# Optimization experiments

Hardware: AMD Instinct MI355X
Metric: run time of the kernel (lower is better)

## Reference

```python
import jax, jax.numpy as jnp
import numpy as np

N_NODES = 100000
N_EDGES = 1600000
N_GRAPHS = 512
NEG_SLOPE = 0.2  # PyG GATConv default


def setup_inputs() -> dict:
    key = jax.random.key(0)
    ks = jax.random.split(key, 12)
    x = jax.random.normal(ks[0], (N_NODES, 75), dtype=jnp.float32)
    edge_index = jax.random.randint(ks[1], (2, N_EDGES), 0, N_NODES, dtype=jnp.int64 if jax.config.jax_enable_x64 else jnp.int32)
    batch = jnp.sort(jax.random.randint(ks[2], (N_NODES,), 0, N_GRAPHS, dtype=jnp.int32))
    s = lambda k, shp, fan: jax.random.normal(k, shp, dtype=jnp.float32) * (1.0 / np.sqrt(fan))
    return {
        "x": x, "edge_index": edge_index, "batch": batch,
        "W1": s(ks[3], (75, 64), 75),           # conv1: heads=8, out=8
        "att_src1": s(ks[4], (8, 8), 8),
        "att_dst1": s(ks[5], (8, 8), 8),
        "bias1": jnp.zeros((64,), jnp.float32),
        "W2": s(ks[6], (64, 128), 64),          # conv2: heads=1, out=128
        "att_src2": s(ks[7], (1, 128), 128),
        "att_dst2": s(ks[8], (1, 128), 128),
        "bias2": jnp.zeros((128,), jnp.float32),
        "Wg": s(ks[9], (128, 1), 128),
        "bg": jnp.zeros((1,), jnp.float32),
    }


def _gat_conv(x, src, dst, W, att_src, att_dst, bias, heads, out_ch):
    # x: [N, F_in]; edges src->dst (self-loops already included)
    n = x.shape[0]
    h = (x @ W).reshape(n, heads, out_ch)            # [N, H, C]
    a_src = (h * att_src).sum(-1)                    # [N, H]
    a_dst = (h * att_dst).sum(-1)                    # [N, H]
    e = a_src[src] + a_dst[dst]                      # [E, H]
    e = jax.nn.leaky_relu(e, NEG_SLOPE)
    # segment softmax over incoming edges of each dst node
    emax = jax.ops.segment_max(e, dst, num_segments=n)      # [N, H]
    ee = jnp.exp(e - emax[dst])
    denom = jax.ops.segment_sum(ee, dst, num_segments=n)    # [N, H]
    alpha = ee / denom[dst]                                  # [E, H]
    msg = h[src] * alpha[:, :, None]                          # [E, H, C]
    out = jax.ops.segment_sum(msg, dst, num_segments=n)      # [N, H, C]
    return out.reshape(n, heads * out_ch) + bias


def reference(x, edge_index, batch, W1, att_src1, att_dst1, bias1,
              W2, att_src2, att_dst2, bias2, Wg, bg):
    n = x.shape[0]
    # PyG GATConv adds self-loops by default
    loops = jnp.arange(n, dtype=edge_index.dtype)
    src = jnp.concatenate([edge_index[0], loops])
    dst = jnp.concatenate([edge_index[1], loops])
    # eval mode: dropout is identity
    x2 = jax.nn.elu(_gat_conv(x, src, dst, W1, att_src1, att_dst1, bias1, heads=8, out_ch=8))
    x4 = _gat_conv(x2, src, dst, W2, att_src2, att_dst2, bias2, heads=1, out_ch=128)
    y = jax.ops.segment_sum(x4, batch, num_segments=N_GRAPHS)  # global_add_pool
    return y @ Wg + bg  # [N_GRAPHS, 1]
```

## Files before the change

### kernel.cpp

```cpp
#include <hip/hip_runtime.h>
#include <hip/hip_bf16.h>
#include <math.h>

#define N_NODES 100000
#define N_EDGES 1600000
#define ET (N_EDGES + N_NODES)
#define N_GRAPHS 512
#define NEG_SLOPE 0.2f
#define G2_BLOCKS 1280

#define BSH 7
#define NDB 128
#define NBUCK ((N_NODES + NDB - 1) / NDB)
#define BCAP 2560
#define ABLK 512
#define CHUNK ((ET + ABLK - 1) / ABLK)
#define F1_OFF (ABLK + 3)
#define PRE_GRID (F1_OFF + 1536)
#define SRC_MASK 131071u

#define BINA_SMEM (CHUNK * 4 + NBUCK * 4 * 4 + 4 + 1024)

__device__ __forceinline__ void atomAddF(float* p, float v) { unsafeAtomicAdd(p, v); }
__device__ __forceinline__ float lrelu(float v) { return v >= 0.f ? v : NEG_SLOPE * v; }

__device__ __forceinline__ unsigned short f2bf(float f) {
    unsigned int u = __float_as_uint(f);
    u += 0x7FFFu + ((u >> 16) & 1u);
    return (unsigned short)(u >> 16);
}
__device__ __forceinline__ float bf2f(unsigned short s) { return __uint_as_float(((unsigned int)s) << 16); }
__device__ __forceinline__ float bflo(unsigned int p) { return __uint_as_float(p << 16); }
__device__ __forceinline__ float bfhi(unsigned int p) { return __uint_as_float(p & 0xFFFF0000u); }

__global__ __launch_bounds__(256) void k_pre(
    const int* __restrict__ ei, unsigned* __restrict__ gbuf, int* __restrict__ bcur,
    const float* __restrict__ x, const float* __restrict__ W1,
    const float* __restrict__ as1, const float* __restrict__ ad1,
    const float* __restrict__ W2, const float* __restrict__ as2,
    const float* __restrict__ ad2, const float* __restrict__ Wg,
    const float* __restrict__ b2, const float* __restrict__ bg,
    unsigned short* __restrict__ h1p, unsigned short* __restrict__ a1sh,
    float* __restrict__ a1d, float* __restrict__ wv, float* __restrict__ out)
{
    __shared__ __align__(16) char smem[BINA_SMEM];
    const int t = threadIdx.x;
    const int blk = blockIdx.x;

    if (blk >= ABLK && blk < F1_OFF) {
        const int bb = blk - ABLK;
        if (bb == 0) {
            if (t < 192) {
                int c = t & 63, which = t >> 6;
                const float* v = (which == 0) ? Wg : ((which == 1) ? as2 : ad2);
                float s = 0.f;
                #pragma unroll
                for (int k = 0; k < 128; ++k) s += W2[c * 128 + k] * v[k];
                wv[which * 64 + c] = s;
            } else if (t == 192) {
                float s = 0.f;
                #pragma unroll
                for (int k = 0; k < 128; ++k) s += b2[k] * Wg[k];
                wv[192] = s;
            }
        } else {
            int i = (bb - 1) * 256 + t;
            if (i < N_GRAPHS) out[i] = bg[0];
        }
        return;
    }

    if (blk >= F1_OFF) {
        float (*xs)[76] = (float (*)[76])smem;
        const int g = t >> 6;
        const int c = t & 63;
        const int vb = blk - F1_OFF;
        const int fstride = PRE_GRID - F1_OFF;
        for (int nb = vb; nb < N_NODES / 4; nb += fstride) {
            const int n = nb * 4 + g;
            const float* xr = x + (long)n * 75;
            xs[g][c] = xr[c];
            if (c < 11) xs[g][64 + c] = xr[64 + c];
            __syncthreads();
            float h = 0.f;
            #pragma unroll
            for (int k = 0; k < 75; ++k) h += xs[g][k] * W1[k * 64 + c];
            h1p[(long)n * 64 + c] = f2bf(h);
            const int head = c >> 3, lane = c & 7;
            float vs = h * as1[c];
            float vd = h * ad1[c];
            #pragma unroll
            for (int off = 1; off < 8; off <<= 1) {
                vs += __shfl_xor(vs, off, 64);
                vd += __shfl_xor(vd, off, 64);
            }
            if (lane == 0) { a1sh[n * 8 + head] = f2bf(vs); a1d[n * 8 + head] = vd; }
            __syncthreads();
        }
        return;
    }

    unsigned* pairs = (unsigned*)smem;
    int* hist  = (int*)(smem + CHUNK * 4);
    int* excl  = hist + NBUCK;
    int* gbase = excl + NBUCK + 1;
    int* cnt2  = gbase + NBUCK;
    int* red   = cnt2 + NBUCK;
    const long e0 = (long)blk * CHUNK;
    const int  n  = (int)((e0 + CHUNK <= ET) ? CHUNK : (ET - e0));
    for (int i = t; i < NBUCK; i += 256) { hist[i] = 0; cnt2[i] = 0; }
    __syncthreads();
    for (int i = t; i < n; i += 256) {
        long e = e0 + i;
        int dst = (e < N_EDGES) ? ei[N_EDGES + e] : (int)(e - N_EDGES);
        atomicAdd(&hist[dst >> BSH], 1);
    }
    __syncthreads();
    {
        int lk[4]; int s = 0;
        #pragma unroll
        for (int k = 0; k < 4; ++k) {
            int idx = t * 4 + k;
            int v = (idx < NBUCK) ? hist[idx] : 0;
            lk[k] = s; s += v;
        }
        red[t] = s;
        __syncthreads();
        for (int off = 1; off < 256; off <<= 1) {
            int a = (t >= off) ? red[t - off] : 0;
            __syncthreads();
            red[t] += a;
            __syncthreads();
        }
        int p = red[t] - s;
        #pragma unroll
        for (int k = 0; k < 4; ++k) {
            int idx = t * 4 + k;
            if (idx < NBUCK) excl[idx] = p + lk[k];
        }
    }
    if (t == 0) excl[NBUCK] = n;
    __syncthreads();
    for (int i = t; i < n; i += 256) {
        long e = e0 + i;
        int src, dst;
        if (e < N_EDGES) { src = ei[e]; dst = ei[N_EDGES + e]; }
        else             { src = dst = (int)(e - N_EDGES); }
        int b = dst >> BSH;
        int pos = excl[b] + atomicAdd(&cnt2[b], 1);
        pairs[pos] = ((unsigned)(dst & (NDB - 1)) << 17) | (unsigned)src;
    }
    __syncthreads();
    for (int b = t; b < NBUCK; b += 256)
        gbase[b] = hist[b] ? atomicAdd(&bcur[b], hist[b]) : 0;
    __syncthreads();
    for (int b = t; b < NBUCK; b += 256) {
        const int s = excl[b], e2 = excl[b + 1];
        if (s == e2) continue;
        unsigned* gp = gbuf + (long)b * BCAP + gbase[b];
        for (int i = s; i < e2; ++i) gp[i - s] = pairs[i];
    }
}

#define SLOT_INIT(k) \
    bool v##k = (k < dgl); \
    int s##k = v##k ? lds_src[beg + k] : 0; \
    unsigned short ab##k = a1sh[(long)s##k * 8 + l]; \
    uint4 pv##k = *(const uint4*)(h1p + (long)s##k * 64 + l * 8);

#define SLOT_STEP(k) { \
    float ee = v##k ? __expf(lrelu(bf2f(ab##k) + adh)) : 0.f; \
    den += ee; \
    acc[0] += ee * bflo(pv##k.x); acc[1] += ee * bfhi(pv##k.x); \
    acc[2] += ee * bflo(pv##k.y); acc[3] += ee * bfhi(pv##k.y); \
    acc[4] += ee * bflo(pv##k.z); acc[5] += ee * bfhi(pv##k.z); \
    acc[6] += ee * bflo(pv##k.w); acc[7] += ee * bfhi(pv##k.w); \
    v##k = (j + 5 + k) < dgl; \
    int sn = v##k ? lds_src[beg + j + 5 + k] : 0; \
    ab##k = a1sh[(long)sn * 8 + l]; \
    pv##k = *(const uint4*)(h1p + (long)sn * 64 + l * 8); }

__global__ __launch_bounds__(512) void k_gat1(
    const unsigned* __restrict__ gbuf, const int* __restrict__ bcur,
    int* __restrict__ rowptr, int* __restrict__ ecol,
    const unsigned short* __restrict__ a1sh, const float* __restrict__ a1d,
    const unsigned short* __restrict__ h1p, const float* __restrict__ bias1,
    const float* __restrict__ wv,
    float2* __restrict__ sg2, float* __restrict__ a2dv)
{
    __shared__ int lds_src[BCAP];
    __shared__ int hist[NDB], excl[NDB + 1], cnt2[NDB];
    __shared__ int red[512];
    const int t = threadIdx.x;
    const int b = blockIdx.x;
    const int d0 = b << BSH;
    const int nloc = (N_NODES - d0 < NDB) ? (N_NODES - d0) : NDB;
    int cntr = bcur[b];
    const int cnt = cntr < BCAP ? cntr : BCAP;

    int partial = 0;
    for (int i = t; i < b; i += 512) partial += bcur[i];
    red[t] = partial;
    __syncthreads();
    for (int off = 256; off > 0; off >>= 1) {
        if (t < off) red[t] += red[t + off];
        __syncthreads();
    }
    const int base = red[0];
    __syncthreads();

    if (t < NDB) { hist[t] = 0; cnt2[t] = 0; }
    __syncthreads();
    const unsigned* eb = gbuf + (long)b * BCAP;
    for (int i = t; i < cnt; i += 512) atomicAdd(&hist[eb[i] >> 17], 1);
    __syncthreads();
    {
        int v = (t < NDB) ? hist[t] : 0;
        if (t < NDB) red[t] = v;
        __syncthreads();
        for (int off = 1; off < NDB; off <<= 1) {
            int a = (t < NDB && t >= off) ? red[t - off] : 0;
            __syncthreads();
            if (t < NDB) red[t] += a;
            __syncthreads();
        }
        if (t < nloc) excl[t] = red[t] - v;
        if (t == 0) excl[nloc] = cnt;
    }
    __syncthreads();
    if (t < nloc) rowptr[d0 + t] = base + excl[t];
    if (b == NBUCK - 1 && t == 0) rowptr[N_NODES] = base + cnt;
    for (int i = t; i < cnt; i += 512) {
        unsigned pr = eb[i];
        int dl = (int)(pr >> 17);
        int slot = excl[dl] + atomicAdd(&cnt2[dl], 1);
        lds_src[slot] = (int)(pr & SRC_MASK);
    }
    __syncthreads();
    for (int i = t; i < cnt; i += 512) ecol[base + i] = lds_src[i];

    const int l = t & 7;
    const int gid = t >> 3;
    for (int dl = gid; dl < nloc; dl += 64) {
        const int dst = d0 + dl;
        const int beg = excl[dl];
        const int dgl = excl[dl + 1] - beg;
        const float adh = a1d[(long)dst * 8 + l];

        float acc[8] = {0.f,0.f,0.f,0.f,0.f,0.f,0.f,0.f};
        float den = 0.f;

        SLOT_INIT(0) SLOT_INIT(1) SLOT_INIT(2) SLOT_INIT(3) SLOT_INIT(4)

        for (int j = 0; j < dgl; j += 5) {
            SLOT_STEP(0) SLOT_STEP(1) SLOT_STEP(2) SLOT_STEP(3) SLOT_STEP(4)
        }

        const float inv = 1.f / den;
        float pg = 0.f, ps = 0.f, pd = 0.f;
        #pragma unroll
        for (int k = 0; k < 8; ++k) {
            float vv = acc[k] * inv + bias1[l * 8 + k];
            vv = vv > 0.f ? vv : (__expf(vv) - 1.f);
            pg += vv * wv[l * 8 + k];
            ps += vv * wv[64 + l * 8 + k];
            pd += vv * wv[128 + l * 8 + k];
        }
        #pragma unroll
        for (int off = 1; off < 8; off <<= 1) {
            pg += __shfl_xor(pg, off, 64);
            ps += __shfl_xor(ps, off, 64);
            pd += __shfl_xor(pd, off, 64);
        }
        if (l == 0) { sg2[dst] = make_float2(ps, pg); a2dv[dst] = pd; }
    }
}

__global__ __launch_bounds__(256) void k_gat2(
    const int* __restrict__ rowptr, const int* __restrict__ ecol,
    const float2* __restrict__ sg2, const float* __restrict__ a2dv,
    const float* __restrict__ wv, const int* __restrict__ batch,
    float* __restrict__ out)
{
    const int sl = threadIdx.x & 7;
    const int sgid = ((blockIdx.x * 256 + threadIdx.x) >> 3);
    const int NS = G2_BLOCKS * 32;
    const int per = (N_NODES + NS - 1) / NS;
    const int n0 = sgid * per;
    const int n1 = min(n0 + per, N_NODES);
    const float bc = wv[192];

    float accg = 0.f;
    int curg = -1;
    for (int n = n0; n < n1; ++n) {
        const int beg = rowptr[n], end = rowptr[n + 1];
        const float adv = a2dv[n];
        float num = 0.f, den = 0.f;
        for (int j = beg + sl; j < end; j += 8) {
            int s = ecol[j];
            float2 v = sg2[s];
            float ee = __expf(lrelu(v.x + adv));
            den += ee;
            num += ee * v.y;
        }
        #pragma unroll
        for (int off = 1; off < 8; off <<= 1) {
            den += __shfl_xor(den, off, 64);
            num += __shfl_xor(num, off, 64);
        }
        if (sl == 0) {
            int gr = batch[n];
            if (gr != curg) {
                if (curg >= 0) atomAddF(out + curg, accg);
                curg = gr; accg = 0.f;
            }
            accg += num / den + bc;
        }
    }
    if (sl == 0 && curg >= 0) atomAddF(out + curg, accg);
}

extern "C" void kernel_launch(void* const* d_in, const int* in_sizes, int n_in,
                              void* d_out, int out_size, void* d_ws, size_t ws_size,
                              hipStream_t stream) {
    (void)in_sizes; (void)n_in; (void)out_size; (void)ws_size;
    const float* x     = (const float*)d_in[0];
    const int*   ei    = (const int*)d_in[1];
    const int*   batch = (const int*)d_in[2];
    const float* W1    = (const float*)d_in[3];
    const float* as1   = (const float*)d_in[4];
    const float* ad1   = (const float*)d_in[5];
    const float* b1    = (const float*)d_in[6];
    const float* W2    = (const float*)d_in[7];
    const float* as2   = (const float*)d_in[8];
    const float* ad2   = (const float*)d_in[9];
    const float* b2    = (const float*)d_in[10];
    const float* Wg    = (const float*)d_in[11];
    const float* bg    = (const float*)d_in[12];
    float* out = (float*)d_out;

    const long N = N_NODES;
    char* p = (char*)d_ws;
    int* rowptr = (int*)p;              p += (N + 4)        * sizeof(int);
    int* bcur   = (int*)p;              p += 1024           * sizeof(int);
    int* ecol   = (int*)p;              p += (long)ET       * sizeof(int);
    unsigned* gbuf = (unsigned*)p;      p += (long)NBUCK * BCAP * sizeof(unsigned);
    unsigned short* h1p  = (unsigned short*)p; p += N * 64  * sizeof(unsigned short);
    unsigned short* a1sh = (unsigned short*)p; p += N * 8   * sizeof(unsigned short);
    float* a1d  = (float*)p;            p += N * 8          * sizeof(float);
    float2* sg2 = (float2*)p;           p += N              * sizeof(float2);
    float* a2dv = (float*)p;            p += N              * sizeof(float);
    float* wv   = (float*)p;            p += 256            * sizeof(float);

    hipMemsetAsync(bcur, 0, NBUCK * sizeof(int), stream);
    k_pre <<<PRE_GRID, 256, 0, stream>>>(ei, gbuf, bcur, x, W1, as1, ad1,
                                         W2, as2, ad2, Wg, b2, bg,
                                         h1p, a1sh, a1d, wv, out);
    k_gat1<<<NBUCK, 512, 0, stream>>>(gbuf, bcur, rowptr, ecol,
                                      a1sh, a1d, h1p, b1, wv, sg2, a2dv);
    k_gat2<<<G2_BLOCKS, 256, 0, stream>>>(rowptr, ecol, sg2, a2dv, wv, batch, out);
}
```

Before: 265.7 us.

## Split CSR build from layer-1 gather, register-tile first linear, widen gat2 groups

```diff
diff --git a/kernel.cpp b/kernel.cpp
--- a/kernel.cpp
+++ b/kernel.cpp
@@ -16,7 +16,8 @@
 #define ABLK 512
 #define CHUNK ((ET + ABLK - 1) / ABLK)
 #define F1_OFF (ABLK + 3)
-#define PRE_GRID (F1_OFF + 1536)
+#define NTILE ((N_NODES + 63) / 64)
+#define PRE_GRID (F1_OFF + NTILE)
 #define SRC_MASK 131071u
 
 #define BINA_SMEM (CHUNK * 4 + NBUCK * 4 * 4 + 4 + 1024)
@@ -71,31 +72,64 @@
     }
 
     if (blk >= F1_OFF) {
-        float (*xs)[76] = (float (*)[76])smem;
-        const int g = t >> 6;
+        float* xs = (float*)smem;
         const int c = t & 63;
+        const int w = t >> 6;
         const int vb = blk - F1_OFF;
         const int fstride = PRE_GRID - F1_OFF;
-        for (int nb = vb; nb < N_NODES / 4; nb += fstride) {
-            const int n = nb * 4 + g;
-            const float* xr = x + (long)n * 75;
-            xs[g][c] = xr[c];
-            if (c < 11) xs[g][64 + c] = xr[64 + c];
-            __syncthreads();
-            float h = 0.f;
+        for (int tile = vb; tile < NTILE; tile += fstride) {
+            const int n0 = tile * 64;
+            const int nv = (N_NODES - n0 < 64) ? (N_NODES - n0) : 64;
+            __syncthreads();
+            const int tot = nv * 75;
+            for (int i = t; i < tot; i += 256) {
+                int nn = i / 75;
+                int kk = i - nn * 75;
+                xs[nn * 76 + kk] = x[(long)n0 * 75 + i];
+            }
+            __syncthreads();
+            const int nb = w * 16;
+            float h[16];
             #pragma unroll
-            for (int k = 0; k < 75; ++k) h += xs[g][k] * W1[k * 64 + c];
-            h1p[(long)n * 64 + c] = f2bf(h);
+            for (int q = 0; q < 16; ++q) h[q] = 0.f;
+            const float* xw = xs + nb * 76;
+            #pragma unroll
+            for (int k4 = 0; k4 < 18; ++k4) {
+                float w0 = W1[(k4 * 4 + 0) * 64 + c];
+                float w1 = W1[(k4 * 4 + 1) * 64 + c];
+                float w2 = W1[(k4 * 4 + 2) * 64 + c];
+                float w3 = W1[(k4 * 4 + 3) * 64 + c];
+                #pragma unroll
+                for (int q = 0; q < 16; ++q) {
+                    float4 xv = *(const float4*)(xw + q * 76 + k4 * 4);
+                    h[q] = fmaf(xv.x, w0, h[q]);
+                    h[q] = fmaf(xv.y, w1, h[q]);
+                    h[q] = fmaf(xv.z, w2, h[q]);
+                    h[q] = fmaf(xv.w, w3, h[q]);
+                }
+            }
+            #pragma unroll
+            for (int k = 72; k < 75; ++k) {
+                float wk = W1[k * 64 + c];
+                #pragma unroll
+                for (int q = 0; q < 16; ++q) h[q] = fmaf(xw[q * 76 + k], wk, h[q]);
+            }
             const int head = c >> 3, lane = c & 7;
-            float vs = h * as1[c];
-            float vd = h * ad1[c];
             #pragma unroll
-            for (int off = 1; off < 8; off <<= 1) {
-                vs += __shfl_xor(vs, off, 64);
-                vd += __shfl_xor(vd, off, 64);
-            }
-            if (lane == 0) { a1sh[n * 8 + head] = f2bf(vs); a1d[n * 8 + head] = vd; }
-            __syncthreads();
+            for (int q = 0; q < 16; ++q) {
+                const int n = n0 + nb + q;
+                if (n < N_NODES) {
+                    h1p[(long)n * 64 + c] = f2bf(h[q]);
+                    float vs = h[q] * as1[c];
+                    float vd = h[q] * ad1[c];
+                    #pragma unroll
+                    for (int off = 1; off < 8; off <<= 1) {
+                        vs += __shfl_xor(vs, off, 64);
+                        vd += __shfl_xor(vd, off, 64);
+                    }
+                    if (lane == 0) { a1sh[n * 8 + head] = f2bf(vs); a1d[n * 8 + head] = vd; }
+                }
+            }
         }
         return;
     }
@@ -162,33 +196,10 @@
     }
 }
 
-#define SLOT_INIT(k) \
-    bool v##k = (k < dgl); \
-    int s##k = v##k ? lds_src[beg + k] : 0; \
-    unsigned short ab##k = a1sh[(long)s##k * 8 + l]; \
-    uint4 pv##k = *(const uint4*)(h1p + (long)s##k * 64 + l * 8);
-
-#define SLOT_STEP(k) { \
-    float ee = v##k ? __expf(lrelu(bf2f(ab##k) + adh)) : 0.f; \
-    den += ee; \
-    acc[0] += ee * bflo(pv##k.x); acc[1] += ee * bfhi(pv##k.x); \
-    acc[2] += ee * bflo(pv##k.y); acc[3] += ee * bfhi(pv##k.y); \
-    acc[4] += ee * bflo(pv##k.z); acc[5] += ee * bfhi(pv##k.z); \
-    acc[6] += ee * bflo(pv##k.w); acc[7] += ee * bfhi(pv##k.w); \
-    v##k = (j + 5 + k) < dgl; \
-    int sn = v##k ? lds_src[beg + j + 5 + k] : 0; \
-    ab##k = a1sh[(long)sn * 8 + l]; \
-    pv##k = *(const uint4*)(h1p + (long)sn * 64 + l * 8); }
-
-__global__ __launch_bounds__(512) void k_gat1(
+__global__ __launch_bounds__(512) void k_build(
     const unsigned* __restrict__ gbuf, const int* __restrict__ bcur,
-    int* __restrict__ rowptr, int* __restrict__ ecol,
-    const unsigned short* __restrict__ a1sh, const float* __restrict__ a1d,
-    const unsigned short* __restrict__ h1p, const float* __restrict__ bias1,
-    const float* __restrict__ wv,
-    float2* __restrict__ sg2, float* __restrict__ a2dv)
+    int* __restrict__ rowptr, int* __restrict__ ecol)
 {
-    __shared__ int lds_src[BCAP];
     __shared__ int hist[NDB], excl[NDB + 1], cnt2[NDB];
     __shared__ int red[512];
     const int t = threadIdx.x;
@@ -234,46 +245,69 @@
         unsigned pr = eb[i];
         int dl = (int)(pr >> 17);
         int slot = excl[dl] + atomicAdd(&cnt2[dl], 1);
-        lds_src[slot] = (int)(pr & SRC_MASK);
-    }
-    __syncthreads();
-    for (int i = t; i < cnt; i += 512) ecol[base + i] = lds_src[i];
-
+        ecol[base + slot] = (int)(pr & SRC_MASK);
+    }
+}
+
+#define GSLOT_INIT(k) \
+    bool v##k = (k < dgl); \
+    int s##k = v##k ? erow[k] : 0; \
+    unsigned short ab##k = a1sh[(long)s##k * 8 + l]; \
+    uint4 pv##k = *(const uint4*)(h1p + (long)s##k * 64 + l * 8);
+
+#define GSLOT_STEP(k) { \
+    float ee = v##k ? __expf(lrelu(bf2f(ab##k) + adh)) : 0.f; \
+    den += ee; \
+    acc[0] += ee * bflo(pv##k.x); acc[1] += ee * bfhi(pv##k.x); \
+    acc[2] += ee * bflo(pv##k.y); acc[3] += ee * bfhi(pv##k.y); \
+    acc[4] += ee * bflo(pv##k.z); acc[5] += ee * bfhi(pv##k.z); \
+    acc[6] += ee * bflo(pv##k.w); acc[7] += ee * bfhi(pv##k.w); \
+    v##k = (j + 3 + k) < dgl; \
+    int sn = v##k ? erow[j + 3 + k] : 0; \
+    ab##k = a1sh[(long)sn * 8 + l]; \
+    pv##k = *(const uint4*)(h1p + (long)sn * 64 + l * 8); }
+
+__global__ __launch_bounds__(256, 6) void k_gath(
+    const int* __restrict__ rowptr, const int* __restrict__ ecol,
+    const unsigned short* __restrict__ a1sh, const float* __restrict__ a1d,
+    const unsigned short* __restrict__ h1p, const float* __restrict__ bias1,
+    const float* __restrict__ wv,
+    float2* __restrict__ sg2, float* __restrict__ a2dv)
+{
+    const int t = threadIdx.x;
     const int l = t & 7;
-    const int gid = t >> 3;
-    for (int dl = gid; dl < nloc; dl += 64) {
-        const int dst = d0 + dl;
-        const int beg = excl[dl];
-        const int dgl = excl[dl + 1] - beg;
-        const float adh = a1d[(long)dst * 8 + l];
-
-        float acc[8] = {0.f,0.f,0.f,0.f,0.f,0.f,0.f,0.f};
-        float den = 0.f;
-
-        SLOT_INIT(0) SLOT_INIT(1) SLOT_INIT(2) SLOT_INIT(3) SLOT_INIT(4)
-
-        for (int j = 0; j < dgl; j += 5) {
-            SLOT_STEP(0) SLOT_STEP(1) SLOT_STEP(2) SLOT_STEP(3) SLOT_STEP(4)
-        }
-
-        const float inv = 1.f / den;
-        float pg = 0.f, ps = 0.f, pd = 0.f;
-        #pragma unroll
-        for (int k = 0; k < 8; ++k) {
-            float vv = acc[k] * inv + bias1[l * 8 + k];
-            vv = vv > 0.f ? vv : (__expf(vv) - 1.f);
-            pg += vv * wv[l * 8 + k];
-            ps += vv * wv[64 + l * 8 + k];
-            pd += vv * wv[128 + l * 8 + k];
-        }
-        #pragma unroll
-        for (int off = 1; off < 8; off <<= 1) {
-            pg += __shfl_xor(pg, off, 64);
-            ps += __shfl_xor(ps, off, 64);
-            pd += __shfl_xor(pd, off, 64);
-        }
-        if (l == 0) { sg2[dst] = make_float2(ps, pg); a2dv[dst] = pd; }
-    }
+    const int dst = (blockIdx.x * 256 + t) >> 3;
+
+    const int beg = rowptr[dst];
+    const int dgl = rowptr[dst + 1] - beg;
+    const int* __restrict__ erow = ecol + beg;
+    const float adh = a1d[(long)dst * 8 + l];
+
+    float acc[8] = {0.f,0.f,0.f,0.f,0.f,0.f,0.f,0.f};
+    float den = 0.f;
+
+    GSLOT_INIT(0) GSLOT_INIT(1) GSLOT_INIT(2)
+    for (int j = 0; j < dgl; j += 3) {
+        GSLOT_STEP(0) GSLOT_STEP(1) GSLOT_STEP(2)
+    }
+
+    const float inv = 1.f / den;
+    float pg = 0.f, ps = 0.f, pd = 0.f;
+    #pragma unroll
+    for (int k = 0; k < 8; ++k) {
+        float vv = acc[k] * inv + bias1[l * 8 + k];
+        vv = vv > 0.f ? vv : (__expf(vv) - 1.f);
+        pg += vv * wv[l * 8 + k];
+        ps += vv * wv[64 + l * 8 + k];
+        pd += vv * wv[128 + l * 8 + k];
+    }
+    #pragma unroll
+    for (int off = 1; off < 8; off <<= 1) {
+        pg += __shfl_xor(pg, off, 64);
+        ps += __shfl_xor(ps, off, 64);
+        pd += __shfl_xor(pd, off, 64);
+    }
+    if (l == 0) { sg2[dst] = make_float2(ps, pg); a2dv[dst] = pd; }
 }
 
 __global__ __launch_bounds__(256) void k_gat2(
@@ -282,9 +316,9 @@
     const float* __restrict__ wv, const int* __restrict__ batch,
     float* __restrict__ out)
 {
-    const int sl = threadIdx.x & 7;
-    const int sgid = ((blockIdx.x * 256 + threadIdx.x) >> 3);
-    const int NS = G2_BLOCKS * 32;
+    const int sl = threadIdx.x & 15;
+    const int sgid = ((blockIdx.x * 256 + threadIdx.x) >> 4);
+    const int NS = G2_BLOCKS * 16;
     const int per = (N_NODES + NS - 1) / NS;
     const int n0 = sgid * per;
     const int n1 = min(n0 + per, N_NODES);
@@ -296,7 +330,7 @@
         const int beg = rowptr[n], end = rowptr[n + 1];
         const float adv = a2dv[n];
         float num = 0.f, den = 0.f;
-        for (int j = beg + sl; j < end; j += 8) {
+        for (int j = beg + sl; j < end; j += 16) {
             int s = ecol[j];
             float2 v = sg2[s];
             float ee = __expf(lrelu(v.x + adv));
@@ -304,7 +338,7 @@
             num += ee * v.y;
         }
         #pragma unroll
-        for (int off = 1; off < 8; off <<= 1) {
+        for (int off = 1; off < 16; off <<= 1) {
             den += __shfl_xor(den, off, 64);
             num += __shfl_xor(num, off, 64);
         }
@@ -356,7 +390,8 @@
     k_pre <<<PRE_GRID, 256, 0, stream>>>(ei, gbuf, bcur, x, W1, as1, ad1,
                                          W2, as2, ad2, Wg, b2, bg,
                                          h1p, a1sh, a1d, wv, out);
-    k_gat1<<<NBUCK, 512, 0, stream>>>(gbuf, bcur, rowptr, ecol,
-                                      a1sh, a1d, h1p, b1, wv, sg2, a2dv);
+    k_build<<<NBUCK, 512, 0, stream>>>(gbuf, bcur, rowptr, ecol);
+    k_gath<<<N_NODES / 32, 256, 0, stream>>>(rowptr, ecol, a1sh, a1d, h1p, b1,
+                                             wv, sg2, a2dv);
     k_gat2<<<G2_BLOCKS, 256, 0, stream>>>(rowptr, ecol, sg2, a2dv, wv, batch, out);
 }
```

Result: slower. 889.3 us (+234.7%).

## Precompute bucket bases in last binning block, shrink gat1 prefetch, widen gat2 lanes

Applied to the files above, without the earlier changes.

```diff
diff --git a/kernel.cpp b/kernel.cpp
--- a/kernel.cpp
+++ b/kernel.cpp
@@ -18,6 +18,7 @@
 #define F1_OFF (ABLK + 3)
 #define PRE_GRID (F1_OFF + 1536)
 #define SRC_MASK 131071u
+#define DONE_SLOT 1023
 
 #define BINA_SMEM (CHUNK * 4 + NBUCK * 4 * 4 + 4 + 1024)
 
@@ -35,6 +36,7 @@
 
 __global__ __launch_bounds__(256) void k_pre(
     const int* __restrict__ ei, unsigned* __restrict__ gbuf, int* __restrict__ bcur,
+    int* __restrict__ bbase,
     const float* __restrict__ x, const float* __restrict__ W1,
     const float* __restrict__ as1, const float* __restrict__ ad1,
     const float* __restrict__ W2, const float* __restrict__ as2,
@@ -160,6 +162,37 @@
         unsigned* gp = gbuf + (long)b * BCAP + gbase[b];
         for (int i = s; i < e2; ++i) gp[i - s] = pairs[i];
     }
+
+    __threadfence();
+    __syncthreads();
+    if (t == 0) red[0] = (atomicAdd(&bcur[DONE_SLOT], 1) == ABLK - 1) ? 1 : 0;
+    __syncthreads();
+    const int amlast = red[0];
+    __syncthreads();
+    if (!amlast) return;
+    {
+        int lk[4]; int s = 0;
+        #pragma unroll
+        for (int k = 0; k < 4; ++k) {
+            int idx = t * 4 + k;
+            int v = (idx < NBUCK) ? bcur[idx] : 0;
+            lk[k] = s; s += v;
+        }
+        red[t] = s;
+        __syncthreads();
+        for (int off = 1; off < 256; off <<= 1) {
+            int a = (t >= off) ? red[t - off] : 0;
+            __syncthreads();
+            red[t] += a;
+            __syncthreads();
+        }
+        int p = red[t] - s;
+        #pragma unroll
+        for (int k = 0; k < 4; ++k) {
+            int idx = t * 4 + k;
+            if (idx < NBUCK) bbase[idx] = p + lk[k];
+        }
+    }
 }
 
 #define SLOT_INIT(k) \
@@ -175,13 +208,14 @@
     acc[2] += ee * bflo(pv##k.y); acc[3] += ee * bfhi(pv##k.y); \
     acc[4] += ee * bflo(pv##k.z); acc[5] += ee * bfhi(pv##k.z); \
     acc[6] += ee * bflo(pv##k.w); acc[7] += ee * bfhi(pv##k.w); \
-    v##k = (j + 5 + k) < dgl; \
-    int sn = v##k ? lds_src[beg + j + 5 + k] : 0; \
+    v##k = (j + 3 + k) < dgl; \
+    int sn = v##k ? lds_src[beg + j + 3 + k] : 0; \
     ab##k = a1sh[(long)sn * 8 + l]; \
     pv##k = *(const uint4*)(h1p + (long)sn * 64 + l * 8); }
 
 __global__ __launch_bounds__(512) void k_gat1(
     const unsigned* __restrict__ gbuf, const int* __restrict__ bcur,
+    const int* __restrict__ bbase,
     int* __restrict__ rowptr, int* __restrict__ ecol,
     const unsigned short* __restrict__ a1sh, const float* __restrict__ a1d,
     const unsigned short* __restrict__ h1p, const float* __restrict__ bias1,
@@ -197,17 +231,7 @@
     const int nloc = (N_NODES - d0 < NDB) ? (N_NODES - d0) : NDB;
     int cntr = bcur[b];
     const int cnt = cntr < BCAP ? cntr : BCAP;
-
-    int partial = 0;
-    for (int i = t; i < b; i += 512) partial += bcur[i];
-    red[t] = partial;
-    __syncthreads();
-    for (int off = 256; off > 0; off >>= 1) {
-        if (t < off) red[t] += red[t + off];
-        __syncthreads();
-    }
-    const int base = red[0];
-    __syncthreads();
+    const int base = bbase[b];
 
     if (t < NDB) { hist[t] = 0; cnt2[t] = 0; }
     __syncthreads();
@@ -250,10 +274,10 @@
         float acc[8] = {0.f,0.f,0.f,0.f,0.f,0.f,0.f,0.f};
         float den = 0.f;
 
-        SLOT_INIT(0) SLOT_INIT(1) SLOT_INIT(2) SLOT_INIT(3) SLOT_INIT(4)
-
-        for (int j = 0; j < dgl; j += 5) {
-            SLOT_STEP(0) SLOT_STEP(1) SLOT_STEP(2) SLOT_STEP(3) SLOT_STEP(4)
+        SLOT_INIT(0) SLOT_INIT(1) SLOT_INIT(2)
+
+        for (int j = 0; j < dgl; j += 3) {
+            SLOT_STEP(0) SLOT_STEP(1) SLOT_STEP(2)
         }
 
         const float inv = 1.f / den;
@@ -282,9 +306,9 @@
     const float* __restrict__ wv, const int* __restrict__ batch,
     float* __restrict__ out)
 {
-    const int sl = threadIdx.x & 7;
-    const int sgid = ((blockIdx.x * 256 + threadIdx.x) >> 3);
-    const int NS = G2_BLOCKS * 32;
+    const int sl = threadIdx.x & 15;
+    const int sgid = ((blockIdx.x * 256 + threadIdx.x) >> 4);
+    const int NS = G2_BLOCKS * 16;
     const int per = (N_NODES + NS - 1) / NS;
     const int n0 = sgid * per;
     const int n1 = min(n0 + per, N_NODES);
@@ -296,7 +320,7 @@
         const int beg = rowptr[n], end = rowptr[n + 1];
         const float adv = a2dv[n];
         float num = 0.f, den = 0.f;
-        for (int j = beg + sl; j < end; j += 8) {
+        for (int j = beg + sl; j < end; j += 16) {
             int s = ecol[j];
             float2 v = sg2[s];
             float ee = __expf(lrelu(v.x + adv));
@@ -304,7 +328,7 @@
             num += ee * v.y;
         }
         #pragma unroll
-        for (int off = 1; off < 8; off <<= 1) {
+        for (int off = 1; off < 16; off <<= 1) {
             den += __shfl_xor(den, off, 64);
             num += __shfl_xor(num, off, 64);
         }
@@ -343,6 +367,7 @@
     char* p = (char*)d_ws;
     int* rowptr = (int*)p;              p += (N + 4)        * sizeof(int);
     int* bcur   = (int*)p;              p += 1024           * sizeof(int);
+    int* bbase  = (int*)p;              p += 1024           * sizeof(int);
     int* ecol   = (int*)p;              p += (long)ET       * sizeof(int);
     unsigned* gbuf = (unsigned*)p;      p += (long)NBUCK * BCAP * sizeof(unsigned);
     unsigned short* h1p  = (unsigned short*)p; p += N * 64  * sizeof(unsigned short);
@@ -352,11 +377,11 @@
     float* a2dv = (float*)p;            p += N              * sizeof(float);
     float* wv   = (float*)p;            p += 256            * sizeof(float);
 
-    hipMemsetAsync(bcur, 0, NBUCK * sizeof(int), stream);
-    k_pre <<<PRE_GRID, 256, 0, stream>>>(ei, gbuf, bcur, x, W1, as1, ad1,
+    hipMemsetAsync(bcur, 0, 1024 * sizeof(int), stream);
+    k_pre <<<PRE_GRID, 256, 0, stream>>>(ei, gbuf, bcur, bbase, x, W1, as1, ad1,
                                          W2, as2, ad2, Wg, b2, bg,
                                          h1p, a1sh, a1d, wv, out);
-    k_gat1<<<NBUCK, 512, 0, stream>>>(gbuf, bcur, rowptr, ecol,
+    k_gat1<<<NBUCK, 512, 0, stream>>>(gbuf, bcur, bbase, rowptr, ecol,
                                       a1sh, a1d, h1p, b1, wv, sg2, a2dv);
     k_gat2<<<G2_BLOCKS, 256, 0, stream>>>(rowptr, ecol, sg2, a2dv, wv, batch, out);
 }
```

After: 339.9 us. 1.28x slower.
